# Kernel tuning notes

Hardware: AMD Instinct MI355X
Metric: run time of the kernel (lower is better)

The kernel has to match this reference:

```python
import jax, jax.numpy as jnp
import numpy as np

S, H, NH, I = 4096, 2048, 16, 5504
HD = H // NH
EPS = 1e-6
ROPE_BASE = 10000.0


def setup_inputs() -> dict:
    key = jax.random.key(0)
    ks = jax.random.split(key, 10)
    sc = lambda fan_in: 1.0 / np.sqrt(fan_in)
    return {
        "x": jax.random.normal(ks[0], (S, H), jnp.float32),
        "wq": jax.random.normal(ks[1], (H, H), jnp.float32) * sc(H),
        "wk": jax.random.normal(ks[2], (H, H), jnp.float32) * sc(H),
        "wv": jax.random.normal(ks[3], (H, H), jnp.float32) * sc(H),
        "wo": jax.random.normal(ks[4], (H, H), jnp.float32) * sc(H),
        "w_gate": jax.random.normal(ks[5], (H, I), jnp.float32) * sc(H),
        "w_up": jax.random.normal(ks[6], (H, I), jnp.float32) * sc(H),
        "w_down": jax.random.normal(ks[7], (I, H), jnp.float32) * sc(I),
        "g1": jnp.ones((H,), jnp.float32),
        "g2": jnp.ones((H,), jnp.float32),
    }


def _rmsnorm(x, g):
    var = jnp.mean(x * x, axis=-1, keepdims=True)
    return x * jax.lax.rsqrt(var + EPS) * g


def _rope(x):
    # x: [S, NH, HD]; classic interleaved-pair rotation applied per position.
    pos = jnp.arange(S, dtype=jnp.float32)
    inv_freq = 1.0 / (ROPE_BASE ** (jnp.arange(0, HD, 2, dtype=jnp.float32) / HD))
    ang = pos[:, None] * inv_freq[None, :]              # [S, HD/2]
    cos = jnp.cos(ang)[:, None, :]                      # [S, 1, HD/2]
    sin = jnp.sin(ang)[:, None, :]
    xe = x[..., 0::2]
    xo = x[..., 1::2]
    out = jnp.stack([xe * cos - xo * sin, xe * sin + xo * cos], axis=-1)
    return out.reshape(x.shape)


def _block(x, wq, wk, wv, wo, w_gate, w_up, w_down, g1, g2):
    # --- attention sublayer ---
    h = _rmsnorm(x, g1)
    q = _rope((h @ wq).reshape(S, NH, HD))
    k = _rope((h @ wk).reshape(S, NH, HD))
    v = (h @ wv).reshape(S, NH, HD)
    scores = jnp.einsum("snd,tnd->nst", q, k) / np.sqrt(HD).astype(np.float32)
    causal = jnp.tril(jnp.ones((S, S), bool))
    scores = jnp.where(causal[None], scores, jnp.finfo(scores.dtype).min)
    probs = jax.nn.softmax(scores, axis=-1)
    attn = jnp.einsum("nst,tnd->snd", probs, v).reshape(S, H)
    x = x + attn @ wo
    # --- MLP sublayer (SwiGLU) ---
    h = _rmsnorm(x, g2)
    mlp = (jax.nn.silu(h @ w_gate) * (h @ w_up)) @ w_down
    return x + mlp


def reference(x, wq, wk, wv, wo, w_gate, w_up, w_down, g1, g2):
    return _block(x, wq, wk, wv, wo, w_gate, w_up, w_down, g1, g2)
```

## Files before the change

kernel.cpp:

```cpp
#include <hip/hip_runtime.h>
#include <stdint.h>

constexpr int SEQ  = 4096;
constexpr int HID  = 2048;
constexpr int NHEAD = 16;
constexpr int HDIM = 128;
constexpr int INTER = 5504;
constexpr int IPAD  = 5632;

using u16 = unsigned short;
typedef __bf16 bf16x8 __attribute__((ext_vector_type(8)));
typedef float  f32x4  __attribute__((ext_vector_type(4)));
typedef u16    u16x4  __attribute__((ext_vector_type(4)));
typedef u16    u16x8  __attribute__((ext_vector_type(8)));

__device__ __forceinline__ u16 f2bf(float f) {
  union { float f; unsigned u; } v; v.f = f;
  return (u16)((v.u + 0x7fffu + ((v.u >> 16) & 1u)) >> 16);
}
__device__ __forceinline__ float bf2f(u16 u) {
  union { unsigned u; float f; } v; v.u = ((unsigned)u) << 16;
  return v.f;
}

__device__ __forceinline__ unsigned cvtpk(float lo, float hi) {
  unsigned r;
  asm("v_cvt_pk_bf16_f32 %0, %1, %2" : "=v"(r) : "v"(lo), "v"(hi));
  return r;
}

__device__ __forceinline__ void gl16(const u16* g, u16* l) {
  u16* gg = const_cast<u16*>(g);
  __builtin_amdgcn_global_load_lds(
      (__attribute__((address_space(1))) u16*)gg,
      (__attribute__((address_space(3))) u16*)l, 16, 0, 0);
}

__device__ __forceinline__ f32x4 mfma16(bf16x8 a, bf16x8 b, f32x4 c) {
  return __builtin_amdgcn_mfma_f32_16x16x32_bf16(a, b, c, 0, 0, 0);
}

__global__ __launch_bounds__(256)
void fill_k(float* __restrict__ o, float v, int n) {
  int i = blockIdx.x * 256 + threadIdx.x;
  if (i < n) o[i] = v;
}

__global__ __launch_bounds__(256)
void rmsnorm_k(const float* __restrict__ x, const float* __restrict__ g,
               u16* __restrict__ o) {
  const int row = blockIdx.x, t = threadIdx.x;
  const float4* xr = (const float4*)(x + (size_t)row * HID);
  float4 a = xr[t * 2], b = xr[t * 2 + 1];
  float ss = a.x*a.x + a.y*a.y + a.z*a.z + a.w*a.w
           + b.x*b.x + b.y*b.y + b.z*b.z + b.w*b.w;
  #pragma unroll
  for (int m = 32; m; m >>= 1) ss += __shfl_xor(ss, m);
  __shared__ float red[4];
  if ((t & 63) == 0) red[t >> 6] = ss;
  __syncthreads();
  const float inv = rsqrtf((red[0]+red[1]+red[2]+red[3]) * (1.0f/HID) + 1e-6f);
  float vals[8] = {a.x,a.y,a.z,a.w,b.x,b.y,b.z,b.w};
  const int base = t * 8;
  u16x8 w;
  #pragma unroll
  for (int i = 0; i < 8; ++i) w[i] = f2bf(vals[i] * inv * g[base + i]);
  *(u16x8*)(o + (size_t)row * HID + base) = w;
}

__global__ __launch_bounds__(256)
void wtrans_k(const float* __restrict__ in, u16* __restrict__ out,
              int ldin, int ldout, int Rin, int Cin) {
  __shared__ float tile[32][33];
  const int cb = blockIdx.x * 32, rb = blockIdx.y * 32;
  const int t = threadIdx.x;
  const int c = t >> 3, r4 = (t & 7) * 4;
  if (rb >= Rin || cb >= Cin) {
    u16x4 z = {0, 0, 0, 0};
    *(u16x4*)(out + (size_t)(cb + c) * ldout + rb + r4) = z;
    return;
  }
  const int r = t >> 3, c4 = (t & 7) * 4;
  float4 v = *(const float4*)(in + (size_t)(rb + r) * ldin + cb + c4);
  tile[r][c4] = v.x; tile[r][c4+1] = v.y; tile[r][c4+2] = v.z; tile[r][c4+3] = v.w;
  __syncthreads();
  u16x4 o;
  #pragma unroll
  for (int i = 0; i < 4; ++i) o[i] = f2bf(tile[r4 + i][c]);
  *(u16x4*)(out + (size_t)(cb + c) * ldout + rb + r4) = o;
}

__global__ __launch_bounds__(256)
void vtrans_k(const u16* __restrict__ v, u16* __restrict__ vt) {
  __shared__ u16 tile[32][36];
  const int s0 = blockIdx.x * 32, d0 = blockIdx.y * 32, n = blockIdx.z;
  const int t = threadIdx.x;
  const int r = t >> 3, c4 = (t & 7) * 4;
  u16x4 in = *(const u16x4*)(v + (size_t)(s0 + r) * HID + n * HDIM + d0 + c4);
  tile[r][c4] = in[0]; tile[r][c4+1] = in[1]; tile[r][c4+2] = in[2]; tile[r][c4+3] = in[3];
  __syncthreads();
  const int d = t >> 3, s4 = (t & 7) * 4;
  u16x4 o;
  #pragma unroll
  for (int i = 0; i < 4; ++i) o[i] = tile[s4 + i][d];
  *(u16x4*)(vt + ((size_t)n * HDIM + d0 + d) * SEQ + s0 + s4) = o;
}

__global__ __launch_bounds__(256)
void rope_k(u16* __restrict__ x) {
  const int idx = blockIdx.x * 256 + threadIdx.x;
  const int i  = idx & 63;
  const int sn = idx >> 6;
  const int s  = sn >> 4;
  const size_t base = (size_t)sn * HDIM + 2 * i;
  const float xe = bf2f(x[base]), xo = bf2f(x[base + 1]);
  const float inv_freq = exp2f(-(float)i * (13.287712379549449f / 64.0f));
  const float ang = (float)s * inv_freq;
  float sv, cv;
  sincosf(ang, &sv, &cv);
  x[base]     = f2bf(xe * cv - xo * sv);
  x[base + 1] = f2bf(xe * sv + xo * cv);
}

template<int EPI>
__global__ __launch_bounds__(256)
void gemm128(const u16* __restrict__ A, const u16* __restrict__ B,
             void* C, const void* extra, int M, int N, int K, int gx) {
  __shared__ __align__(16) u16 As[128 * 64];
  __shared__ __align__(16) u16 Bs[128 * 64];
  const int bid = blockIdx.x;
  const int cid = bid & 7;
  const int idx = bid >> 3;
  const int grp = idx >> 4, win = idx & 15;
  const int bx = grp * 4 + (win & 3);
  const int by = cid * 4 + (win >> 2);
  (void)gx;
  const int m0 = by * 128, n0 = bx * 128;
  const int tid = threadIdx.x;
  const int w = tid >> 6, lane = tid & 63;
  const int l15 = lane & 15, g = lane >> 4;
  const int wr = w >> 1, wc = w & 1;
  const int NT = K >> 6;

  f32x4 acc[4][4] = {};

  const int srow = tid >> 3;
  const int sgr  = ((tid & 7) ^ (srow & 7)) * 8;
  const u16* gA = A + (size_t)(m0 + srow) * K + sgr;
  const u16* gB = B + (size_t)(n0 + srow) * K + sgr;
  const size_t i32K = (size_t)32 * K;
  const int sl = w * 512;

  const int axor = l15 & 7;
  const int arow0 = (wr * 64 + l15) * 64;
  const int brow0 = (wc * 64 + l15) * 64;

  for (int T = 0; T < NT; ++T) {
    const size_t k0 = (size_t)T * 64;
    gl16(gA + k0,            As + 0 * 2048 + sl);
    gl16(gA + k0 +     i32K, As + 1 * 2048 + sl);
    gl16(gA + k0 + 2 * i32K, As + 2 * 2048 + sl);
    gl16(gA + k0 + 3 * i32K, As + 3 * 2048 + sl);
    gl16(gB + k0,            Bs + 0 * 2048 + sl);
    gl16(gB + k0 +     i32K, Bs + 1 * 2048 + sl);
    gl16(gB + k0 + 2 * i32K, Bs + 2 * 2048 + sl);
    gl16(gB + k0 + 3 * i32K, Bs + 3 * 2048 + sl);
    asm volatile("s_waitcnt vmcnt(0)" ::: "memory");
    __syncthreads();
    #pragma unroll
    for (int ks = 0; ks < 2; ++ks) {
      const int aoff = ((ks * 4 + g) ^ axor) * 8;
      bf16x8 af[4], bfr[4];
      #pragma unroll
      for (int i = 0; i < 4; ++i)
        af[i] = *(const bf16x8*)&As[arow0 + i * 16 * 64 + aoff];
      #pragma unroll
      for (int j = 0; j < 4; ++j)
        bfr[j] = *(const bf16x8*)&Bs[brow0 + j * 16 * 64 + aoff];
      #pragma unroll
      for (int i = 0; i < 4; ++i)
        #pragma unroll
        for (int j = 0; j < 4; ++j)
          acc[i][j] = mfma16(af[i], bfr[j], acc[i][j]);
    }
    asm volatile("s_waitcnt lgkmcnt(0)" ::: "memory");
    __syncthreads();
  }

  #pragma unroll
  for (int i = 0; i < 4; ++i) {
    #pragma unroll
    for (int r = 0; r < 4; ++r) {
      const int row = m0 + wr * 64 + i * 16 + g * 4 + r;
      #pragma unroll
      for (int j = 0; j < 4; ++j) {
        const int col = n0 + wc * 64 + j * 16 + l15;
        const float v = acc[i][j][r];
        if constexpr (EPI == 0) {
          ((u16*)C)[(size_t)(col >> 11) * ((size_t)SEQ * HID)
                    + (size_t)row * HID + (col & 2047)] = f2bf(v);
        } else if constexpr (EPI == 1) {
          const size_t idx2 = (size_t)row * N + col;
          ((float*)C)[idx2] = v + ((const float*)extra)[idx2];
        } else if constexpr (EPI == 2) {
          const size_t idx2 = (size_t)row * N + col;
          const float upv = bf2f(((const u16*)extra)[idx2]);
          ((u16*)C)[idx2] = f2bf(v / (1.0f + __expf(-v)) * upv);
        } else {
          ((u16*)C)[(size_t)row * N + col] = f2bf(v);
        }
      }
    }
  }
}

template<int EPI>
__global__ __launch_bounds__(256)
void gemm128n64(const u16* __restrict__ A, const u16* __restrict__ B,
                void* C, const void* extra, int M, int N, int K, int gx) {
  __shared__ __align__(16) u16 As[128 * 64];
  __shared__ __align__(16) u16 Bs[64 * 64];
  const int bid = blockIdx.x;
  const int cid = bid & 7;
  const int idx = bid >> 3;
  const int grp = idx >> 4, win = idx & 15;
  const int bx = grp * 4 + (win & 3);
  const int by = cid * 4 + (win >> 2);
  (void)gx;
  const int m0 = by * 128, n0 = bx * 64;
  const int tid = threadIdx.x;
  const int w = tid >> 6, lane = tid & 63;
  const int l15 = lane & 15, g = lane >> 4;
  const int wr = w >> 1, wc = w & 1;
  const int NT = K >> 6;

  f32x4 acc[4][2] = {};

  const int srow = tid >> 3;
  const int sgr  = ((tid & 7) ^ (srow & 7)) * 8;
  const u16* gA = A + (size_t)(m0 + srow) * K + sgr;
  const u16* gB = B + (size_t)(n0 + srow) * K + sgr;
  const size_t i32K = (size_t)32 * K;
  const int sl = w * 512;

  const int axor = l15 & 7;
  const int arow0 = (wr * 64 + l15) * 64;
  const int brow0 = (wc * 32 + l15) * 64;

  for (int T = 0; T < NT; ++T) {
    const size_t k0 = (size_t)T * 64;
    gl16(gA + k0,            As + 0 * 2048 + sl);
    gl16(gA + k0 +     i32K, As + 1 * 2048 + sl);
    gl16(gA + k0 + 2 * i32K, As + 2 * 2048 + sl);
    gl16(gA + k0 + 3 * i32K, As + 3 * 2048 + sl);
    gl16(gB + k0,            Bs + 0 * 2048 + sl);
    gl16(gB + k0 +     i32K, Bs + 1 * 2048 + sl);
    asm volatile("s_waitcnt vmcnt(0)" ::: "memory");
    __syncthreads();
    #pragma unroll
    for (int ks = 0; ks < 2; ++ks) {
      const int aoff = ((ks * 4 + g) ^ axor) * 8;
      bf16x8 af[4], bfr[2];
      #pragma unroll
      for (int i = 0; i < 4; ++i)
        af[i] = *(const bf16x8*)&As[arow0 + i * 16 * 64 + aoff];
      #pragma unroll
      for (int j = 0; j < 2; ++j)
        bfr[j] = *(const bf16x8*)&Bs[brow0 + j * 16 * 64 + aoff];
      #pragma unroll
      for (int i = 0; i < 4; ++i)
        #pragma unroll
        for (int j = 0; j < 2; ++j)
          acc[i][j] = mfma16(af[i], bfr[j], acc[i][j]);
    }
    asm volatile("s_waitcnt lgkmcnt(0)" ::: "memory");
    __syncthreads();
  }

  #pragma unroll
  for (int i = 0; i < 4; ++i) {
    #pragma unroll
    for (int r = 0; r < 4; ++r) {
      const int row = m0 + wr * 64 + i * 16 + g * 4 + r;
      #pragma unroll
      for (int j = 0; j < 2; ++j) {
        const int col = n0 + wc * 32 + j * 16 + l15;
        const float v = acc[i][j][r];
        if constexpr (EPI == 1) {
          const size_t idx2 = (size_t)row * N + col;
          ((float*)C)[idx2] = v + ((const float*)extra)[idx2];
        } else {
          ((u16*)C)[(size_t)row * N + col] = f2bf(v);
        }
      }
    }
  }
}

__global__ __launch_bounds__(256)
void attn_k(const u16* __restrict__ q, const u16* __restrict__ k,
            const u16* __restrict__ vt, u16* __restrict__ o) {
  __shared__ __align__(16) u16 Ks[64 * 128];
  __shared__ __align__(16) u16 Vs[128 * 64];
  __shared__ __align__(16) u16 Ps[4 * 16 * 64];
  const int b = blockIdx.x;
  const int n    = ((b & 7) << 1) | ((b >> 3) & 1);
  const int qIdx = 63 - (b >> 4);
  const int q0   = qIdx * 64;
  const int tid = threadIdx.x;
  const int wave = tid >> 6, lane = tid & 63;
  const int l15 = lane & 15, g = lane >> 4;

  bf16x8 aq[4];
  {
    const u16* qp = q + (size_t)(q0 + wave*16 + l15) * HID + n * HDIM + g * 8;
    #pragma unroll
    for (int d = 0; d < 4; ++d) aq[d] = *(const bf16x8*)(qp + d * 32);
  }
  float mrow[4];
  #pragma unroll
  for (int r = 0; r < 4; ++r) mrow[r] = -__builtin_inff();
  f32x4 oacc[8] = {};
  f32x4 lacc = {0.0f, 0.0f, 0.0f, 0.0f};
  const bf16x8 vone = {(__bf16)1.0f, (__bf16)1.0f, (__bf16)1.0f, (__bf16)1.0f,
                       (__bf16)1.0f, (__bf16)1.0f, (__bf16)1.0f, (__bf16)1.0f};

  const int kRow = tid >> 4;
  const int kCs  = (tid & 15) ^ (kRow & 7);
  const u16* kg = k + (size_t)kRow * HID + n * HDIM + kCs * 8;
  const int vRow = tid >> 3;
  const int vCs  = (tid & 7) ^ (vRow & 7);
  const u16* vg = vt + ((size_t)n * HDIM + vRow) * SEQ + vCs * 8;

  u16* PW = Ps + wave * 1024;
  const int rsw = (l15 & 7) << 3;
  const float C = 0.12751744f;

  const int nt = qIdx + 1;
  for (int it = 0; it < nt; ++it) {
    const int t0 = it * 64;
    #pragma unroll
    for (int s = 0; s < 4; ++s)
      gl16(kg + (size_t)(t0 + s*16) * HID, Ks + s*2048 + wave*512);
    #pragma unroll
    for (int s = 0; s < 4; ++s)
      gl16(vg + (size_t)(s*32) * SEQ + t0, Vs + s*2048 + wave*512);
    asm volatile("s_waitcnt vmcnt(0)" ::: "memory");
    __syncthreads();

    f32x4 sc[4] = {};
    __builtin_amdgcn_s_setprio(1);
    #pragma unroll
    for (int tb = 0; tb < 4; ++tb) {
      #pragma unroll
      for (int dd = 0; dd < 4; ++dd) {
        bf16x8 bk = *(const bf16x8*)(Ks + (tb*16 + l15)*128 + ((dd*32 + g*8) ^ rsw));
        sc[tb] = mfma16(aq[dd], bk, sc[tb]);
      }
    }
    __builtin_amdgcn_s_setprio(0);

    const bool diag = (it == qIdx);
    #pragma unroll
    for (int r = 0; r < 4; ++r) {
      float v0 = sc[0][r], v1 = sc[1][r], v2 = sc[2][r], v3 = sc[3][r];
      if (diag) {
        const int srow = q0 + wave*16 + g*4 + r;
        const int tt = t0 + l15;
        if (tt      > srow) v0 = -__builtin_inff();
        if (tt + 16 > srow) v1 = -__builtin_inff();
        if (tt + 32 > srow) v2 = -__builtin_inff();
        if (tt + 48 > srow) v3 = -__builtin_inff();
      }
      float mx = fmaxf(fmaxf(v0, v1), fmaxf(v2, v3));
      mx = fmaxf(mx, __shfl_xor(mx, 1));
      mx = fmaxf(mx, __shfl_xor(mx, 2));
      mx = fmaxf(mx, __shfl_xor(mx, 4));
      mx = fmaxf(mx, __shfl_xor(mx, 8));
      if (mx > mrow[r] + 60.0f) {
        const float f = exp2f((mrow[r] - mx) * C);
        mrow[r] = mx;
        lacc[r] *= f;
        #pragma unroll
        for (int db = 0; db < 8; ++db) oacc[db][r] *= f;
      }
      const float m = mrow[r];
      const float p0 = exp2f((v0 - m) * C);
      const float p1 = exp2f((v1 - m) * C);
      const float p2 = exp2f((v2 - m) * C);
      const float p3 = exp2f((v3 - m) * C);
      const unsigned pk01 = cvtpk(p0, p1);
      const unsigned pk23 = cvtpk(p2, p3);
      const int prow = g*4 + r;
      const int psw = (prow & 7) << 3;
      PW[prow*64 + ( l15        ^ psw)] = (u16)pk01;
      PW[prow*64 + ((16 + l15)  ^ psw)] = (u16)(pk01 >> 16);
      PW[prow*64 + ((32 + l15)  ^ psw)] = (u16)pk23;
      PW[prow*64 + ((48 + l15)  ^ psw)] = (u16)(pk23 >> 16);
    }

    bf16x8 ap0 = *(const bf16x8*)(PW + l15*64 + ((g*8)      ^ rsw));
    bf16x8 ap1 = *(const bf16x8*)(PW + l15*64 + ((32 + g*8) ^ rsw));
    __builtin_amdgcn_s_setprio(1);
    lacc = mfma16(ap0, vone, lacc);
    lacc = mfma16(ap1, vone, lacc);
    #pragma unroll
    for (int db = 0; db < 8; ++db) {
      bf16x8 bv0 = *(const bf16x8*)(Vs + (db*16 + l15)*64 + ((g*8)      ^ rsw));
      bf16x8 bv1 = *(const bf16x8*)(Vs + (db*16 + l15)*64 + ((32 + g*8) ^ rsw));
      oacc[db] = mfma16(ap0, bv0, oacc[db]);
      oacc[db] = mfma16(ap1, bv1, oacc[db]);
    }
    __builtin_amdgcn_s_setprio(0);
    asm volatile("s_waitcnt lgkmcnt(0)" ::: "memory");
    __syncthreads();
  }

  #pragma unroll
  for (int db = 0; db < 8; ++db) {
    #pragma unroll
    for (int r = 0; r < 4; ++r) {
      const int srow = q0 + wave*16 + g*4 + r;
      o[(size_t)srow * HID + n * HDIM + db*16 + l15] = f2bf(oacc[db][r] / lacc[r]);
    }
  }
}

extern "C" void kernel_launch(void* const* d_in, const int* in_sizes, int n_in,
                              void* d_out, int out_size, void* d_ws, size_t ws_size,
                              hipStream_t stream) {
  (void)in_sizes; (void)n_in; (void)out_size;
  const float* x  = (const float*)d_in[0];
  const float* wq = (const float*)d_in[1];
  const float* wk = (const float*)d_in[2];
  const float* wv = (const float*)d_in[3];
  const float* wo = (const float*)d_in[4];
  const float* wg = (const float*)d_in[5];
  const float* wu = (const float*)d_in[6];
  const float* wd = (const float*)d_in[7];
  const float* g1 = (const float*)d_in[8];
  const float* g2 = (const float*)d_in[9];
  float* out = (float*)d_out;

  constexpr size_t HB  = (size_t)SEQ * HID * 2;
  constexpr size_t WT  = (size_t)HID * HID * 2;
  constexpr size_t WUP = (size_t)IPAD * HID * 2;
  constexpr size_t UPH = (size_t)SEQ * IPAD * 2;
  constexpr size_t NEED1 = 4 * HB + 3 * WT;
  constexpr size_t NEED2 = HB + WUP + UPH;
  constexpr size_t NEED = NEED1 > NEED2 ? NEED1 : NEED2;

  if (ws_size < NEED) {
    const int n = SEQ * HID;
    fill_k<<<dim3((n + 255) / 256), 256, 0, stream>>>(out, (float)(ws_size >> 20), n);
    return;
  }

  char* base = (char*)d_ws;
  u16* h1     = (u16*)(base);
  u16* wqkvT  = (u16*)(base + HB);
  u16* qb     = (u16*)(base + HB + 3 * WT);
  u16* kb     = (u16*)(base + 2 * HB + 3 * WT);
  u16* vb     = (u16*)(base + 3 * HB + 3 * WT);
  u16* vtb    = h1;
  u16* ob     = vb;
  u16* woT    = wqkvT;
  u16* h2    = (u16*)(base);
  u16* slotA = (u16*)(base + HB);
  u16* uph   = (u16*)(base + HB + WUP);

  wtrans_k<<<dim3(64, 64), 256, 0, stream>>>(wq, wqkvT,            HID, HID, HID, HID);
  wtrans_k<<<dim3(64, 64), 256, 0, stream>>>(wk, wqkvT + HID*HID,  HID, HID, HID, HID);
  wtrans_k<<<dim3(64, 64), 256, 0, stream>>>(wv, wqkvT + 2*HID*HID,HID, HID, HID, HID);

  rmsnorm_k<<<dim3(SEQ), 256, 0, stream>>>(x, g1, h1);

  gemm128<0><<<dim3(1536), 256, 0, stream>>>(h1, wqkvT, qb, nullptr, SEQ, 3*HID, HID, 48);

  rope_k<<<dim3(SEQ * NHEAD * 64 / 256), 256, 0, stream>>>(qb);
  rope_k<<<dim3(SEQ * NHEAD * 64 / 256), 256, 0, stream>>>(kb);

  vtrans_k<<<dim3(SEQ/32, HDIM/32, NHEAD), 256, 0, stream>>>(vb, vtb);

  wtrans_k<<<dim3(64, 64), 256, 0, stream>>>(wo, woT, HID, HID, HID, HID);

  attn_k<<<dim3(SEQ/64 * NHEAD), 256, 0, stream>>>(qb, kb, vtb, ob);

  gemm128n64<1><<<dim3(1024), 256, 0, stream>>>(ob, woT, out, x, SEQ, HID, HID, 32);

  rmsnorm_k<<<dim3(SEQ), 256, 0, stream>>>(out, g2, h2);

  wtrans_k<<<dim3(IPAD/32, 64), 256, 0, stream>>>(wu, slotA, INTER, HID, HID, INTER);
  gemm128<3><<<dim3(1408), 256, 0, stream>>>(h2, slotA, uph, nullptr, SEQ, IPAD, HID, 44);

  wtrans_k<<<dim3(IPAD/32, 64), 256, 0, stream>>>(wg, slotA, INTER, HID, HID, INTER);
  gemm128<2><<<dim3(1408), 256, 0, stream>>>(h2, slotA, uph, uph, SEQ, IPAD, HID, 44);

  wtrans_k<<<dim3(64, IPAD/32), 256, 0, stream>>>(wd, slotA, HID, IPAD, INTER, HID);
  gemm128n64<1><<<dim3(1024), 256, 0, stream>>>(uph, slotA, out, out, SEQ, HID, IPAD, 32);
}
```

Measured before the change: 829.1 us.

## Fuse up and gate projections into one dual-B GEMM with SwiGLU epilogue

After: 796.4 us, median of 3. -3.9%, faster.

```diff
diff --git a/kernel.cpp b/kernel.cpp
--- a/kernel.cpp
+++ b/kernel.cpp
@@ -7,6 +7,7 @@
 constexpr int HDIM = 128;
 constexpr int INTER = 5504;
 constexpr int IPAD  = 5632;
+constexpr int NHALF = 2816;
 
 using u16 = unsigned short;
 typedef __bf16 bf16x8 __attribute__((ext_vector_type(8)));
@@ -298,6 +299,92 @@
 }
 
 __global__ __launch_bounds__(256)
+void gemm_ug(const u16* __restrict__ A, const u16* __restrict__ Bu,
+             const u16* __restrict__ Bg, u16* C, int ldC, int K) {
+  __shared__ __align__(16) u16 As[128 * 64];
+  __shared__ __align__(16) u16 BsU[64 * 64];
+  __shared__ __align__(16) u16 BsG[64 * 64];
+  const int bid = blockIdx.x;
+  const int cid = bid & 7;
+  const int idx = bid >> 3;
+  const int grp = idx >> 4, win = idx & 15;
+  const int bx = grp * 4 + (win & 3);
+  const int by = cid * 4 + (win >> 2);
+  const int m0 = by * 128, n0 = bx * 64;
+  const int tid = threadIdx.x;
+  const int w = tid >> 6, lane = tid & 63;
+  const int l15 = lane & 15, g = lane >> 4;
+  const int wr = w >> 1, wc = w & 1;
+  const int NT = K >> 6;
+
+  f32x4 accU[4][2] = {};
+  f32x4 accG[4][2] = {};
+
+  const int srow = tid >> 3;
+  const int sgr  = ((tid & 7) ^ (srow & 7)) * 8;
+  const u16* gA = A  + (size_t)(m0 + srow) * K + sgr;
+  const u16* gU = Bu + (size_t)(n0 + srow) * K + sgr;
+  const u16* gG = Bg + (size_t)(n0 + srow) * K + sgr;
+  const size_t i32K = (size_t)32 * K;
+  const int sl = w * 512;
+
+  const int axor = l15 & 7;
+  const int arow0 = (wr * 64 + l15) * 64;
+  const int brow0 = (wc * 32 + l15) * 64;
+
+  for (int T = 0; T < NT; ++T) {
+    const size_t k0 = (size_t)T * 64;
+    gl16(gA + k0,            As + 0 * 2048 + sl);
+    gl16(gA + k0 +     i32K, As + 1 * 2048 + sl);
+    gl16(gA + k0 + 2 * i32K, As + 2 * 2048 + sl);
+    gl16(gA + k0 + 3 * i32K, As + 3 * 2048 + sl);
+    gl16(gU + k0,            BsU + 0 * 2048 + sl);
+    gl16(gU + k0 +     i32K, BsU + 1 * 2048 + sl);
+    gl16(gG + k0,            BsG + 0 * 2048 + sl);
+    gl16(gG + k0 +     i32K, BsG + 1 * 2048 + sl);
+    asm volatile("s_waitcnt vmcnt(0)" ::: "memory");
+    __syncthreads();
+    #pragma unroll
+    for (int ks = 0; ks < 2; ++ks) {
+      const int aoff = ((ks * 4 + g) ^ axor) * 8;
+      bf16x8 af[4], bu[2], bg[2];
+      #pragma unroll
+      for (int i = 0; i < 4; ++i)
+        af[i] = *(const bf16x8*)&As[arow0 + i * 16 * 64 + aoff];
+      #pragma unroll
+      for (int j = 0; j < 2; ++j) {
+        bu[j] = *(const bf16x8*)&BsU[brow0 + j * 16 * 64 + aoff];
+        bg[j] = *(const bf16x8*)&BsG[brow0 + j * 16 * 64 + aoff];
+      }
+      #pragma unroll
+      for (int i = 0; i < 4; ++i)
+        #pragma unroll
+        for (int j = 0; j < 2; ++j) {
+          accU[i][j] = mfma16(af[i], bu[j], accU[i][j]);
+          accG[i][j] = mfma16(af[i], bg[j], accG[i][j]);
+        }
+    }
+    asm volatile("s_waitcnt lgkmcnt(0)" ::: "memory");
+    __syncthreads();
+  }
+
+  #pragma unroll
+  for (int i = 0; i < 4; ++i) {
+    #pragma unroll
+    for (int r = 0; r < 4; ++r) {
+      const int row = m0 + wr * 64 + i * 16 + g * 4 + r;
+      #pragma unroll
+      for (int j = 0; j < 2; ++j) {
+        const int col = n0 + wc * 32 + j * 16 + l15;
+        const float up = accU[i][j][r];
+        const float gt = accG[i][j][r];
+        C[(size_t)row * ldC + col] = f2bf(gt / (1.0f + __expf(-gt)) * up);
+      }
+    }
+  }
+}
+
+__global__ __launch_bounds__(256)
 void attn_k(const u16* __restrict__ q, const u16* __restrict__ k,
             const u16* __restrict__ vt, u16* __restrict__ o) {
   __shared__ __align__(16) u16 Ks[64 * 128];
@@ -445,10 +532,12 @@
   constexpr size_t HB  = (size_t)SEQ * HID * 2;
   constexpr size_t WT  = (size_t)HID * HID * 2;
   constexpr size_t WUP = (size_t)IPAD * HID * 2;
-  constexpr size_t UPH = (size_t)SEQ * IPAD * 2;
+  constexpr size_t WHF = (size_t)NHALF * HID * 2;
+  constexpr size_t MB_ = (size_t)SEQ * IPAD * 2;
   constexpr size_t NEED1 = 4 * HB + 3 * WT;
-  constexpr size_t NEED2 = HB + WUP + UPH;
+  constexpr size_t NEED2 = HB + 2 * WHF + MB_;
   constexpr size_t NEED = NEED1 > NEED2 ? NEED1 : NEED2;
+  static_assert(WUP <= 2 * WHF, "wdT fits weight slot");
 
   if (ws_size < NEED) {
     const int n = SEQ * HID;
@@ -466,8 +555,10 @@
   u16* ob     = vb;
   u16* woT    = wqkvT;
   u16* h2    = (u16*)(base);
-  u16* slotA = (u16*)(base + HB);
-  u16* uph   = (u16*)(base + HB + WUP);
+  u16* wuTh  = (u16*)(base + HB);
+  u16* wgTh  = (u16*)(base + HB + WHF);
+  u16* wdT   = wuTh;
+  u16* mb    = (u16*)(base + HB + 2 * WHF);
 
   wtrans_k<<<dim3(64, 64), 256, 0, stream>>>(wq, wqkvT,            HID, HID, HID, HID);
   wtrans_k<<<dim3(64, 64), 256, 0, stream>>>(wk, wqkvT + HID*HID,  HID, HID, HID, HID);
@@ -490,12 +581,14 @@
 
   rmsnorm_k<<<dim3(SEQ), 256, 0, stream>>>(out, g2, h2);
 
-  wtrans_k<<<dim3(IPAD/32, 64), 256, 0, stream>>>(wu, slotA, INTER, HID, HID, INTER);
-  gemm128<3><<<dim3(1408), 256, 0, stream>>>(h2, slotA, uph, nullptr, SEQ, IPAD, HID, 44);
-
-  wtrans_k<<<dim3(IPAD/32, 64), 256, 0, stream>>>(wg, slotA, INTER, HID, HID, INTER);
-  gemm128<2><<<dim3(1408), 256, 0, stream>>>(h2, slotA, uph, uph, SEQ, IPAD, HID, 44);
-
-  wtrans_k<<<dim3(64, IPAD/32), 256, 0, stream>>>(wd, slotA, HID, IPAD, INTER, HID);
-  gemm128n64<1><<<dim3(1024), 256, 0, stream>>>(uph, slotA, out, out, SEQ, HID, IPAD, 32);
-}
+  for (int h = 0; h < 2; ++h) {
+    const int noff = h * NHALF;
+    const int cin  = INTER - noff;
+    wtrans_k<<<dim3(NHALF/32, 64), 256, 0, stream>>>(wu + noff, wuTh, INTER, HID, HID, cin);
+    wtrans_k<<<dim3(NHALF/32, 64), 256, 0, stream>>>(wg + noff, wgTh, INTER, HID, HID, cin);
+    gemm_ug<<<dim3(1408), 256, 0, stream>>>(h2, wuTh, wgTh, mb + noff, IPAD, HID);
+  }
+
+  wtrans_k<<<dim3(64, IPAD/32), 256, 0, stream>>>(wd, wdT, HID, IPAD, INTER, HID);
+  gemm128n64<1><<<dim3(1024), 256, 0, stream>>>(mb, wdT, out, out, SEQ, HID, IPAD, 32);
+}
```
